# Performance work log

Hardware: AMD Instinct MI355X
Metric: run time of the kernel (lower is better)

The kernel has to match this reference:

```python
import jax, jax.numpy as jnp
import numpy as np

N_EMBD = 1024
N_HEAD = 16
HEAD_DIM = N_EMBD // N_HEAD  # 64
R = 8
D_STD = HEAD_DIM - R         # 56
BLOCK_SIZE = 2048
B, T = 2, 2048
NEG = -1e9


def setup_inputs() -> dict:
    key = jax.random.key(0)
    ks = jax.random.split(key, 8)
    x = jax.random.normal(ks[0], (B, T, N_EMBD), dtype=jnp.float32)
    Wqkv = jax.random.normal(ks[1], (3 * N_EMBD, N_EMBD), dtype=jnp.float32) * 0.02
    Wproj = jax.random.normal(ks[2], (N_EMBD, N_EMBD), dtype=jnp.float32) * 0.02
    W_recip = jax.random.normal(ks[3], (HEAD_DIM, R), dtype=jnp.float32) * 0.02
    # mixing weights must be positive (sqrt is taken); match init scale
    w_std = jnp.full((N_HEAD,), 0.5, dtype=jnp.float32)
    w_rec = jnp.full((N_HEAD,), 0.3, dtype=jnp.float32)  # > threshold -> all heads RA
    w_disc = jnp.full((N_HEAD,), 0.2, dtype=jnp.float32)
    d_bias = jax.random.normal(ks[4], (N_HEAD, BLOCK_SIZE), dtype=jnp.float32) * 0.02
    return {"x": x, "Wqkv": Wqkv, "Wproj": Wproj, "W_recip": W_recip,
            "w_std": w_std, "w_rec": w_rec, "w_disc": w_disc, "d_bias": d_bias}


def reference(x, Wqkv, Wproj, W_recip, w_std, w_rec, w_disc, d_bias):
    Bx, Tx, C = x.shape
    H, hd = N_HEAD, HEAD_DIM
    qkv = x @ Wqkv.T                                   # (B,T,3C)
    q, k, v = jnp.split(qkv, 3, axis=-1)
    def heads(t):
        return t.reshape(Bx, Tx, H, hd).transpose(0, 2, 1, 3)  # (B,H,T,hd)
    q, k, v = heads(q), heads(k), heads(v)
    q_low = jnp.einsum('bhtd,dr->bhtr', q, W_recip)    # (B,H,T,R)
    k_low = jnp.einsum('bhtd,dr->bhtr', k, W_recip)
    sw_std = jnp.sqrt(w_std)[None, :, None, None]
    sw_rec = jnp.sqrt(w_rec)[None, :, None, None]
    # cross augmentation: q side carries k_low, k side carries q_low
    q_aug = jnp.concatenate([sw_std * q[..., :D_STD], sw_rec * k_low], axis=-1)
    k_aug = jnp.concatenate([sw_std * k[..., :D_STD], sw_rec * q_low], axis=-1)
    scale = 1.0 / jnp.sqrt(jnp.asarray(hd, dtype=x.dtype))
    scores = jnp.einsum('bhqd,bhkd->bhqk', q_aug, k_aug) * scale
    # per-head learned bias over key positions, broadcast over queries
    bias = w_disc[None, :, None, None] * d_bias[:, :Tx][None, :, None, :]
    scores = scores + bias
    causal = jnp.tril(jnp.ones((Tx, Tx), dtype=bool))
    scores = jnp.where(causal[None, None], scores, NEG)
    attn = jax.nn.softmax(scores, axis=-1)
    out = jnp.einsum('bhqk,bhkd->bhqd', attn, v)       # (B,H,T,hd)
    out = out.transpose(0, 2, 1, 3).reshape(Bx, Tx, C)
    return out @ Wproj.T
```

## Files before the change

kernel.cpp:

```cpp
#include <hip/hip_runtime.h>
#include <math.h>

#define T_SEQ 2048
#define NH 16
#define HD 64
#define CEMB 1024
#define NEGINF -3.0e38f
#define LOG2E 1.4426950408889634f

typedef unsigned short ushort;
typedef unsigned int uint;
typedef __attribute__((ext_vector_type(8))) short short8;
typedef __attribute__((ext_vector_type(4))) float f32x4;

#if __has_builtin(__builtin_amdgcn_exp2f)
#define EXP2(x) __builtin_amdgcn_exp2f(x)
#else
#define EXP2(x) exp2f(x)
#endif

__device__ __forceinline__ float b2f(ushort h) {
    union { uint u; float f; } cv; cv.u = ((uint)h) << 16; return cv.f;
}
__device__ __forceinline__ ushort f2b(float f) {
    union { float f; uint u; } cv; cv.f = f;
    return (ushort)((cv.u + 0x7FFF + ((cv.u >> 16) & 1)) >> 16);
}
__device__ __forceinline__ ushort f2b_fast(float f) {
    union { float f; uint u; } cv; cv.f = f;
    return (ushort)((cv.u + 0x8000) >> 16);
}
__device__ __forceinline__ uint pack_bf16(float a, float b) {
    union { float f; uint u; } ua, ub; ua.f = a; ub.f = b;
    return __builtin_amdgcn_perm(ub.u + 0x8000u, ua.u + 0x8000u, 0x07060302u);
}
__device__ __forceinline__ void gl2lds16(const ushort* g, ushort* l) {
    __builtin_amdgcn_global_load_lds(
        (const __attribute__((address_space(1))) void*)g,
        (__attribute__((address_space(3))) void*)l, 16, 0, 0);
}

__global__ __launch_bounds__(256) void prep_kernel(
    const float* __restrict__ x, const float* __restrict__ Wqkv,
    const float* __restrict__ Wproj, const float* __restrict__ W_recip,
    const float* __restrict__ w_disc, const float* __restrict__ d_bias,
    ushort* __restrict__ xb, ushort* __restrict__ wqkvb,
    ushort* __restrict__ wprojb, float* __restrict__ bias_pre)
{
    const int bid = blockIdx.x;
    if (bid < 8192) {
        const float* src; ushort* dst; int off;
        if (bid < 4096)      { src = x;     dst = xb;     off = bid; }
        else if (bid < 7168) { src = Wqkv;  dst = wqkvb;  off = bid - 4096; }
        else                 { src = Wproj; dst = wprojb; off = bid - 7168; }
        const int i = (off * 256 + threadIdx.x) * 4;
        const float4 v = *(const float4*)&src[i];
        ushort4 o;
        o.x = f2b(v.x); o.y = f2b(v.y); o.z = f2b(v.z); o.w = f2b(v.w);
        *(ushort4*)&dst[i] = o;
        return;
    }
    if (bid >= 8224) {
        const int h = bid - 8224;
        const float wd = w_disc[h] * LOG2E;
        const int j = h * T_SEQ + threadIdx.x * 8;
        const float4 a = *(const float4*)&d_bias[j];
        const float4 c = *(const float4*)&d_bias[j + 4];
        float4 oa, oc;
        oa.x = a.x * wd; oa.y = a.y * wd; oa.z = a.z * wd; oa.w = a.w * wd;
        oc.x = c.x * wd; oc.y = c.y * wd; oc.z = c.z * wd; oc.w = c.w * wd;
        *(float4*)&bias_pre[j] = oa;
        *(float4*)&bias_pre[j + 4] = oc;
        return;
    }
    const int wb = bid - 8192;
    const int qk = wb >> 4, h = wb & 15;
    const int e0 = threadIdx.x * 4;
    f32x4 acc[8];
    #pragma unroll
    for (int r = 0; r < 8; ++r) acc[r] = (f32x4){0.f, 0.f, 0.f, 0.f};
    #pragma unroll 4
    for (int d = 0; d < 64; ++d) {
        const float4 xv = *(const float4*)&Wqkv[(size_t)(qk * 1024 + h * 64 + d) * 1024 + e0];
        #pragma unroll
        for (int r = 0; r < 8; ++r) {
            const float w = W_recip[d * 8 + r];
            acc[r][0] = fmaf(w, xv.x, acc[r][0]);
            acc[r][1] = fmaf(w, xv.y, acc[r][1]);
            acc[r][2] = fmaf(w, xv.z, acc[r][2]);
            acc[r][3] = fmaf(w, xv.w, acc[r][3]);
        }
    }
    #pragma unroll
    for (int r = 0; r < 8; ++r) {
        ushort4 o;
        o.x = f2b(acc[r][0]); o.y = f2b(acc[r][1]);
        o.z = f2b(acc[r][2]); o.w = f2b(acc[r][3]);
        *(ushort4*)&wqkvb[(size_t)(3072 + qk * 128 + h * 8 + r) * 1024 + e0] = o;
    }
}

#define GEMM_CORE(Aptr, Bptr, KDIM, SMEMN)                                     \
    __shared__ __align__(16) ushort SMEM[SMEMN];                               \
    ushort* const Asl = SMEM;                                                  \
    ushort* const Bsl = SMEM + 8192;                                           \
    const int row0 = blockIdx.x * 128;                                         \
    const int col0 = blockIdx.y * 128;                                         \
    const int tid = threadIdx.x;                                               \
    const int wave = tid >> 6, lane = tid & 63;                                \
    const int wm = wave >> 1, wn = wave & 1;                                   \
    const int quad = lane >> 4, lq = lane & 15;                                \
    const int l7 = lq & 7;                                                     \
    f32x4 acc[4][4];                                                           \
    _Pragma("unroll") for (int i = 0; i < 4; ++i)                              \
        _Pragma("unroll") for (int j = 0; j < 4; ++j)                          \
            acc[i][j] = (f32x4){0.f, 0.f, 0.f, 0.f};                           \
    for (int k0 = 0; k0 < (KDIM); k0 += 64) {                                  \
        _Pragma("unroll") for (int p = 0; p < 4; ++p) {                        \
            const int idx = p * 256 + tid;                                     \
            const int row = idx >> 3, slot = idx & 7;                          \
            const int kc = (slot ^ (row & 7)) << 3;                            \
            gl2lds16(&(Aptr)[(size_t)(row0 + row) * (KDIM) + k0 + kc], &Asl[idx * 8]); \
            gl2lds16(&(Bptr)[(size_t)(col0 + row) * (KDIM) + k0 + kc], &Bsl[idx * 8]); \
        }                                                                      \
        __syncthreads();                                                       \
        _Pragma("unroll") for (int ks = 0; ks < 2; ++ks) {                     \
            short8 af[4], bf[4];                                               \
            _Pragma("unroll") for (int i = 0; i < 4; ++i)                      \
                af[i] = *(const short8*)&Asl[(wm * 64 + i * 16 + lq) * 64 +    \
                                             (((ks * 4 + quad) ^ l7) << 3)];   \
            _Pragma("unroll") for (int j = 0; j < 4; ++j)                      \
                bf[j] = *(const short8*)&Bsl[(wn * 64 + j * 16 + lq) * 64 +    \
                                             (((ks * 4 + quad) ^ l7) << 3)];   \
            _Pragma("unroll") for (int i = 0; i < 4; ++i)                      \
                _Pragma("unroll") for (int j = 0; j < 4; ++j)                  \
                    acc[i][j] = __builtin_amdgcn_mfma_f32_16x16x32_bf16(       \
                        af[i], bf[j], acc[i][j], 0, 0, 0);                     \
        }                                                                      \
        __syncthreads();                                                       \
    }

__global__ __launch_bounds__(256, 4) void gemm_qkv_kernel(
    const ushort* __restrict__ A, const ushort* __restrict__ Bt,
    const float* __restrict__ w_std, const float* __restrict__ w_rec,
    ushort* __restrict__ qh, ushort* __restrict__ kh, ushort* __restrict__ vt)
{
    GEMM_CORE(A, Bt, 1024, 128 * 136)
    ushort* const Cs = SMEM;

    if (col0 >= 2048 && col0 < 3072) {
        #pragma unroll
        for (int j = 0; j < 4; ++j) {
            const int cc = col0 + wn * 64 + j * 16 + lq;
            const int h = (cc >> 6) & 15;
            const int d = cc & 63;
            #pragma unroll
            for (int i = 0; i < 4; ++i) {
                const int rr0 = row0 + wm * 64 + i * 16 + quad * 4;
                const int b = rr0 >> 11, t0 = rr0 & 2047;
                ushort4 pv;
                pv.x = f2b(acc[i][j][0]); pv.y = f2b(acc[i][j][1]);
                pv.z = f2b(acc[i][j][2]); pv.w = f2b(acc[i][j][3]);
                *(ushort4*)&vt[((((size_t)b * NH + h) * HD + d) * T_SEQ + t0)] = pv;
            }
        }
    } else if (col0 < 2048) {
        const bool isq = (col0 < 1024);
        #pragma unroll
        for (int j = 0; j < 4; ++j) {
            const int colc = wn * 64 + j * 16 + lq;
            const int h = ((col0 + colc) >> 6) & 15;
            const float sc = isq ? w_std[h] * (0.125f * LOG2E) : 1.0f;
            #pragma unroll
            for (int i = 0; i < 4; ++i)
                #pragma unroll
                for (int r = 0; r < 4; ++r)
                    Cs[(wm * 64 + i * 16 + quad * 4 + r) * 136 + colc] =
                        f2b(acc[i][j][r] * sc);
        }
        __syncthreads();
        ushort* dst = isq ? qh : kh;
        const int hbase = (col0 >> 6) & 15;
        #pragma unroll
        for (int rep = 0; rep < 8; ++rep) {
            const int id = rep * 256 + tid;
            const int row = id >> 4, chunk = id & 15;
            if ((chunk & 7) == 7) continue;
            const int h = hbase + (chunk >> 3);
            const int d = (chunk & 7) * 8;
            const int rr = row0 + row;
            const int b = rr >> 11, t = rr & 2047;
            const uint4 val = *(const uint4*)&Cs[row * 136 + chunk * 8];
            *(uint4*)&dst[((((size_t)b * NH + h) * T_SEQ + t) * HD + d)] = val;
        }
    } else {
        const bool isqlow = (col0 < 3200);
        #pragma unroll
        for (int j = 0; j < 4; ++j) {
            const int colc = wn * 64 + j * 16 + lq;
            const int h = colc >> 3;
            const float sc = isqlow ? 1.0f : w_rec[h] * (0.125f * LOG2E);
            #pragma unroll
            for (int i = 0; i < 4; ++i)
                #pragma unroll
                for (int r = 0; r < 4; ++r)
                    Cs[(wm * 64 + i * 16 + quad * 4 + r) * 136 + colc] =
                        f2b(acc[i][j][r] * sc);
        }
        __syncthreads();
        ushort* dst = isqlow ? kh : qh;
        #pragma unroll
        for (int rep = 0; rep < 8; ++rep) {
            const int id = rep * 256 + tid;
            const int row = id >> 4, h = id & 15;
            const int rr = row0 + row;
            const int b = rr >> 11, t = rr & 2047;
            const uint4 val = *(const uint4*)&Cs[row * 136 + h * 8];
            *(uint4*)&dst[((((size_t)b * NH + h) * T_SEQ + t) * HD + 56)] = val;
        }
    }
}

__global__ __launch_bounds__(256, 4) void gemm_proj_kernel(
    const ushort* __restrict__ A, const ushort* __restrict__ Bt,
    float* __restrict__ C)
{
    GEMM_CORE(A, Bt, 1024, 16384)
    #pragma unroll
    for (int i = 0; i < 4; ++i) {
        #pragma unroll
        for (int r = 0; r < 4; ++r) {
            const int rr = row0 + wm * 64 + i * 16 + quad * 4 + r;
            #pragma unroll
            for (int j = 0; j < 4; ++j) {
                const int cc = col0 + wn * 64 + j * 16 + lq;
                C[(size_t)rr * 1024 + cc] = acc[i][j][r];
            }
        }
    }
}

#define TILE_COMPUTE(bq, o4, lsum, qrow, NTL) do {                            \
    f32x4 s4[8];                                                              \
    _Pragma("unroll") for (int nt = 0; nt < (NTL); ++nt)                      \
        s4[nt] = *(const f32x4*)&bias_h[k0 + nt * 16 + quad * 4];             \
    _Pragma("unroll") for (int ks = 0; ks < 2; ++ks)                          \
        _Pragma("unroll") for (int nt = 0; nt < (NTL); ++nt) {                \
            const short8 ak = *(const short8*)                                \
                &Ks[(nt * 16 + lq) * 64 + (((ks * 4 + quad) ^ l7) << 3)];     \
            s4[nt] = __builtin_amdgcn_mfma_f32_16x16x32_bf16(                 \
                ak, (bq)[ks], s4[nt], 0, 0, 0);                               \
        }                                                                     \
    _Pragma("unroll") for (int nt = 0; nt < (NTL); ++nt) {                    \
        f32x4 sv = s4[nt];                                                    \
        const int kb = k0 + nt * 16 + quad * 4;                               \
        _Pragma("unroll") for (int r = 0; r < 4; ++r)                         \
            if (kb + r > (qrow)) sv[r] = NEGINF;                              \
        const float p0 = EXP2(sv[0]), p1 = EXP2(sv[1]);                       \
        const float p2 = EXP2(sv[2]), p3 = EXP2(sv[3]);                       \
        (lsum) += (p0 + p1) + (p2 + p3);                                      \
        const int pcol = (nt * 16 + quad * 4) ^ (l7 << 3);                    \
        uint2 pv; pv.x = pack_bf16(p0, p1); pv.y = pack_bf16(p2, p3);         \
        *(uint2*)&Ps[prow + pcol] = pv;                                       \
    }                                                                         \
    _Pragma("unroll") for (int ks = 0; ks < (NTL) / 2; ++ks) {                \
        const short8 bp = *(const short8*)                                    \
            &Ps[prow + ((ks * 32 + quad * 8) ^ (l7 << 3))];                   \
        _Pragma("unroll") for (int dt = 0; dt < 4; ++dt) {                    \
            const short8 av = *(const short8*)                                \
                &Vs[(dt * 16 + lq) * 128 + (((ks * 4 + quad) ^ lq) << 3)];    \
            (o4)[dt] = __builtin_amdgcn_mfma_f32_16x16x32_bf16(               \
                av, bp, (o4)[dt], 0, 0, 0);                                   \
        }                                                                     \
    }                                                                         \
} while (0)

__global__ __launch_bounds__(256, 2) void attn_kernel(
    const ushort* __restrict__ qa, const ushort* __restrict__ ka,
    const ushort* __restrict__ vt, const float* __restrict__ bias_pre,
    ushort* __restrict__ out)
{
    __shared__ __align__(16) ushort Qs[2 * 64 * 64];
    __shared__ __align__(16) ushort Ks[128 * 64];
    __shared__ __align__(16) ushort Ps[64 * 128];
    __shared__ __align__(16) ushort Vs[64 * 128];
    const int bh = blockIdx.x;
    const int qtA = blockIdx.y;
    const int qtB = 31 - blockIdx.y;
    const int h = bh & 15, b = bh >> 4;
    const int tid = threadIdx.x;
    const int wave = tid >> 6, lane = tid & 63;
    const int quad = lane >> 4, lq = lane & 15;
    const int l7 = lq & 7;
    const size_t base = (size_t)bh * T_SEQ * HD;

    #pragma unroll
    for (int rep = 0; rep < 2; ++rep) {
        const int idx = rep * 256 + tid;
        const int row = idx >> 3, slot = idx & 7;
        const int kc = (slot ^ (row & 7)) << 3;
        gl2lds16(&qa[base + (size_t)(qtA * 64 + row) * 64 + kc], &Qs[idx * 8]);
        gl2lds16(&qa[base + (size_t)(qtB * 64 + row) * 64 + kc], &Qs[4096 + idx * 8]);
    }
    __syncthreads();
    short8 bqA[2], bqB[2];
    #pragma unroll
    for (int ks = 0; ks < 2; ++ks) {
        const int off = (wave * 16 + lq) * 64 + (((ks * 4 + quad) ^ l7) << 3);
        bqA[ks] = *(const short8*)&Qs[off];
        bqB[ks] = *(const short8*)&Qs[4096 + off];
    }

    f32x4 o4A[4], o4B[4];
    #pragma unroll
    for (int dt = 0; dt < 4; ++dt) {
        o4A[dt] = (f32x4){0.f, 0.f, 0.f, 0.f};
        o4B[dt] = (f32x4){0.f, 0.f, 0.f, 0.f};
    }
    float lsumA = 0.f, lsumB = 0.f;
    const int qrowA = qtA * 64 + wave * 16 + lq;
    const int qrowB = qtB * 64 + wave * 16 + lq;
    const int prow = (wave * 16 + lq) * 128;
    const int nA = (qtA + 2) >> 1, nB = (qtB + 2) >> 1;
    const float* bias_h = &bias_pre[h * T_SEQ];

    for (int c = 0; c < nB; ++c) {
        const int k0 = c * 128;
        if (c) __syncthreads();
        #pragma unroll
        for (int rep = 0; rep < 4; ++rep) {
            const int idx = rep * 256 + tid;
            const int row = idx >> 3, slot = idx & 7;
            gl2lds16(&ka[base + (size_t)(k0 + row) * 64 + ((slot ^ (row & 7)) << 3)],
                     &Ks[idx * 8]);
        }
        #pragma unroll
        for (int rep = 0; rep < 4; ++rep) {
            const int idx = rep * 256 + tid;
            const int row = idx >> 4, slot = idx & 15;
            gl2lds16(&vt[base + (size_t)row * T_SEQ + k0 + ((slot ^ (row & 15)) << 3)],
                     &Vs[idx * 8]);
        }
        __syncthreads();

        if (c == nB - 1 && !(qtB & 1)) TILE_COMPUTE(bqB, o4B, lsumB, qrowB, 4);
        else                           TILE_COMPUTE(bqB, o4B, lsumB, qrowB, 8);
        if (c < nA) {
            if (c == nA - 1 && !(qtA & 1)) TILE_COMPUTE(bqA, o4A, lsumA, qrowA, 4);
            else                           TILE_COMPUTE(bqA, o4A, lsumA, qrowA, 8);
        }
    }

    lsumA += __shfl_xor(lsumA, 16, 64);
    lsumA += __shfl_xor(lsumA, 32, 64);
    lsumB += __shfl_xor(lsumB, 16, 64);
    lsumB += __shfl_xor(lsumB, 32, 64);
    const float invA = 1.0f / lsumA, invB = 1.0f / lsumB;
    const size_t obaseA = ((size_t)b * T_SEQ + qrowA) * CEMB + h * HD;
    const size_t obaseB = ((size_t)b * T_SEQ + qrowB) * CEMB + h * HD;
    #pragma unroll
    for (int dt = 0; dt < 4; ++dt) {
        ushort4 ov;
        ov.x = f2b_fast(o4A[dt][0] * invA);
        ov.y = f2b_fast(o4A[dt][1] * invA);
        ov.z = f2b_fast(o4A[dt][2] * invA);
        ov.w = f2b_fast(o4A[dt][3] * invA);
        *(ushort4*)&out[obaseA + dt * 16 + quad * 4] = ov;
        ushort4 ow;
        ow.x = f2b_fast(o4B[dt][0] * invB);
        ow.y = f2b_fast(o4B[dt][1] * invB);
        ow.z = f2b_fast(o4B[dt][2] * invB);
        ow.w = f2b_fast(o4B[dt][3] * invB);
        *(ushort4*)&out[obaseB + dt * 16 + quad * 4] = ow;
    }
}

extern "C" void kernel_launch(void* const* d_in, const int* in_sizes, int n_in,
                              void* d_out, int out_size, void* d_ws, size_t ws_size,
                              hipStream_t stream) {
    const float* x       = (const float*)d_in[0];
    const float* Wqkv    = (const float*)d_in[1];
    const float* Wproj   = (const float*)d_in[2];
    const float* W_recip = (const float*)d_in[3];
    const float* w_std   = (const float*)d_in[4];
    const float* w_rec   = (const float*)d_in[5];
    const float* w_disc  = (const float*)d_in[6];
    const float* d_bias  = (const float*)d_in[7];
    float* out = (float*)d_out;

    const size_t NX = (size_t)4096 * 1024;
    const size_t NWQKVX = (size_t)3328 * 1024;
    const size_t NWPROJ = (size_t)1024 * 1024;
    ushort* xb     = (ushort*)d_ws;
    ushort* wqkvb  = xb + NX;
    ushort* wprojb = wqkvb + NWQKVX;
    ushort* qh     = wprojb + NWPROJ;
    ushort* kh     = qh + NX;
    ushort* vt     = kh + NX;
    ushort* ao     = vt + NX;
    float*  bias_pre = (float*)(ao + NX);

    prep_kernel<<<8240, 256, 0, stream>>>(x, Wqkv, Wproj, W_recip, w_disc, d_bias,
                                          xb, wqkvb, wprojb, bias_pre);
    gemm_qkv_kernel<<<dim3(32, 26), 256, 0, stream>>>(xb, wqkvb, w_std, w_rec, qh, kh, vt);
    attn_kernel<<<dim3(32, 16), 256, 0, stream>>>(qh, kh, vt, bias_pre, ao);
    gemm_proj_kernel<<<dim3(32, 8), 256, 0, stream>>>(ao, wprojb, out);
}
```

Before: 190.7 us.

## Interleave dual query-tile attention compute, drop Q LDS staging, raise occupancy

Restructures the attention inner loop so both paired query tiles (A and B) share each K and V fragment read from LDS, interleaving their MFMAs. It adds s_setprio around the MFMA phases, loads Q directly from global into registers instead of staging through LDS, and reuses the K buffer for A's probabilities after a barrier. Removing the Q buffer frees LDS and launch bounds go from 2 to 3 blocks per SM. The costs are higher register pressure from two sets of score accumulators and one extra barrier per chunk.

```diff
diff --git a/kernel.cpp b/kernel.cpp
--- a/kernel.cpp
+++ b/kernel.cpp
@@ -240,19 +240,9 @@
     }
 }
 
-#define TILE_COMPUTE(bq, o4, lsum, qrow, NTL) do {                            \
-    f32x4 s4[8];                                                              \
-    _Pragma("unroll") for (int nt = 0; nt < (NTL); ++nt)                      \
-        s4[nt] = *(const f32x4*)&bias_h[k0 + nt * 16 + quad * 4];             \
-    _Pragma("unroll") for (int ks = 0; ks < 2; ++ks)                          \
-        _Pragma("unroll") for (int nt = 0; nt < (NTL); ++nt) {                \
-            const short8 ak = *(const short8*)                                \
-                &Ks[(nt * 16 + lq) * 64 + (((ks * 4 + quad) ^ l7) << 3)];     \
-            s4[nt] = __builtin_amdgcn_mfma_f32_16x16x32_bf16(                 \
-                ak, (bq)[ks], s4[nt], 0, 0, 0);                               \
-        }                                                                     \
+#define SOFTMAX_ROWS(sarr, NTL, qrow, lsum, Pdst) do {                        \
     _Pragma("unroll") for (int nt = 0; nt < (NTL); ++nt) {                    \
-        f32x4 sv = s4[nt];                                                    \
+        f32x4 sv = (sarr)[nt];                                                \
         const int kb = k0 + nt * 16 + quad * 4;                               \
         _Pragma("unroll") for (int r = 0; r < 4; ++r)                         \
             if (kb + r > (qrow)) sv[r] = NEGINF;                              \
@@ -261,29 +251,88 @@
         (lsum) += (p0 + p1) + (p2 + p3);                                      \
         const int pcol = (nt * 16 + quad * 4) ^ (l7 << 3);                    \
         uint2 pv; pv.x = pack_bf16(p0, p1); pv.y = pack_bf16(p2, p3);         \
-        *(uint2*)&Ps[prow + pcol] = pv;                                       \
+        *(uint2*)&(Pdst)[prow + pcol] = pv;                                   \
     }                                                                         \
+} while (0)
+
+#define CHUNK_DUAL(NTA) do {                                                  \
+    f32x4 sA[(NTA)], sB[8];                                                   \
+    _Pragma("unroll") for (int nt = 0; nt < 8; ++nt) {                        \
+        const f32x4 bv = *(const f32x4*)&bias_h[k0 + nt * 16 + quad * 4];     \
+        sB[nt] = bv;                                                          \
+        if (nt < (NTA)) sA[nt] = bv;                                          \
+    }                                                                         \
+    __builtin_amdgcn_s_setprio(1);                                            \
+    _Pragma("unroll") for (int ks = 0; ks < 2; ++ks)                          \
+        _Pragma("unroll") for (int nt = 0; nt < 8; ++nt) {                    \
+            const short8 ak = *(const short8*)                                \
+                &Ks[(nt * 16 + lq) * 64 + (((ks * 4 + quad) ^ l7) << 3)];     \
+            sB[nt] = __builtin_amdgcn_mfma_f32_16x16x32_bf16(                 \
+                ak, bqB[ks], sB[nt], 0, 0, 0);                                \
+            if (nt < (NTA))                                                   \
+                sA[nt] = __builtin_amdgcn_mfma_f32_16x16x32_bf16(             \
+                    ak, bqA[ks], sA[nt], 0, 0, 0);                            \
+        }                                                                     \
+    __builtin_amdgcn_s_setprio(0);                                            \
+    __syncthreads();        \
+    SOFTMAX_ROWS(sB, 8, qrowB, lsumB, Ps);                                    \
+    SOFTMAX_ROWS(sA, (NTA), qrowA, lsumA, PA);                                \
+    __builtin_amdgcn_s_setprio(1);                                            \
+    _Pragma("unroll") for (int ks = 0; ks < 4; ++ks) {                        \
+        const int poff = prow + ((ks * 32 + quad * 8) ^ (l7 << 3));           \
+        const short8 bpB = *(const short8*)&Ps[poff];                         \
+        short8 bpA = bpB;                                                     \
+        if (ks < (NTA) / 2) bpA = *(const short8*)&PA[poff];                  \
+        _Pragma("unroll") for (int dt = 0; dt < 4; ++dt) {                    \
+            const short8 av = *(const short8*)                                \
+                &Vs[(dt * 16 + lq) * 128 + (((ks * 4 + quad) ^ lq) << 3)];    \
+            o4B[dt] = __builtin_amdgcn_mfma_f32_16x16x32_bf16(                \
+                av, bpB, o4B[dt], 0, 0, 0);                                   \
+            if (ks < (NTA) / 2)                                               \
+                o4A[dt] = __builtin_amdgcn_mfma_f32_16x16x32_bf16(            \
+                    av, bpA, o4A[dt], 0, 0, 0);                               \
+        }                                                                     \
+    }                                                                         \
+    __builtin_amdgcn_s_setprio(0);                                            \
+} while (0)
+
+#define CHUNK_SINGLE(NTL) do {                                                \
+    f32x4 sB[(NTL)];                                                          \
+    _Pragma("unroll") for (int nt = 0; nt < (NTL); ++nt)                      \
+        sB[nt] = *(const f32x4*)&bias_h[k0 + nt * 16 + quad * 4];             \
+    __builtin_amdgcn_s_setprio(1);                                            \
+    _Pragma("unroll") for (int ks = 0; ks < 2; ++ks)                          \
+        _Pragma("unroll") for (int nt = 0; nt < (NTL); ++nt) {                \
+            const short8 ak = *(const short8*)                                \
+                &Ks[(nt * 16 + lq) * 64 + (((ks * 4 + quad) ^ l7) << 3)];     \
+            sB[nt] = __builtin_amdgcn_mfma_f32_16x16x32_bf16(                 \
+                ak, bqB[ks], sB[nt], 0, 0, 0);                                \
+        }                                                                     \
+    __builtin_amdgcn_s_setprio(0);                                            \
+    SOFTMAX_ROWS(sB, (NTL), qrowB, lsumB, Ps);                                \
+    __builtin_amdgcn_s_setprio(1);                                            \
     _Pragma("unroll") for (int ks = 0; ks < (NTL) / 2; ++ks) {                \
-        const short8 bp = *(const short8*)                                    \
+        const short8 bpB = *(const short8*)                                   \
             &Ps[prow + ((ks * 32 + quad * 8) ^ (l7 << 3))];                   \
         _Pragma("unroll") for (int dt = 0; dt < 4; ++dt) {                    \
             const short8 av = *(const short8*)                                \
                 &Vs[(dt * 16 + lq) * 128 + (((ks * 4 + quad) ^ lq) << 3)];    \
-            (o4)[dt] = __builtin_amdgcn_mfma_f32_16x16x32_bf16(               \
-                av, bp, (o4)[dt], 0, 0, 0);                                   \
+            o4B[dt] = __builtin_amdgcn_mfma_f32_16x16x32_bf16(                \
+                av, bpB, o4B[dt], 0, 0, 0);                                   \
         }                                                                     \
     }                                                                         \
+    __builtin_amdgcn_s_setprio(0);                                            \
 } while (0)
 
-__global__ __launch_bounds__(256, 2) void attn_kernel(
+__global__ __launch_bounds__(256, 3) void attn_kernel(
     const ushort* __restrict__ qa, const ushort* __restrict__ ka,
     const ushort* __restrict__ vt, const float* __restrict__ bias_pre,
     ushort* __restrict__ out)
 {
-    __shared__ __align__(16) ushort Qs[2 * 64 * 64];
     __shared__ __align__(16) ushort Ks[128 * 64];
     __shared__ __align__(16) ushort Ps[64 * 128];
     __shared__ __align__(16) ushort Vs[64 * 128];
+    ushort* const PA = Ks;
     const int bh = blockIdx.x;
     const int qtA = blockIdx.y;
     const int qtB = 31 - blockIdx.y;
@@ -294,21 +343,15 @@
     const int l7 = lq & 7;
     const size_t base = (size_t)bh * T_SEQ * HD;
 
-    #pragma unroll
-    for (int rep = 0; rep < 2; ++rep) {
-        const int idx = rep * 256 + tid;
-        const int row = idx >> 3, slot = idx & 7;
-        const int kc = (slot ^ (row & 7)) << 3;
-        gl2lds16(&qa[base + (size_t)(qtA * 64 + row) * 64 + kc], &Qs[idx * 8]);
-        gl2lds16(&qa[base + (size_t)(qtB * 64 + row) * 64 + kc], &Qs[4096 + idx * 8]);
-    }
-    __syncthreads();
+    const int qrowA = qtA * 64 + wave * 16 + lq;
+    const int qrowB = qtB * 64 + wave * 16 + lq;
+
     short8 bqA[2], bqB[2];
     #pragma unroll
     for (int ks = 0; ks < 2; ++ks) {
-        const int off = (wave * 16 + lq) * 64 + (((ks * 4 + quad) ^ l7) << 3);
-        bqA[ks] = *(const short8*)&Qs[off];
-        bqB[ks] = *(const short8*)&Qs[4096 + off];
+        const int dq = (ks * 4 + quad) * 8;
+        bqA[ks] = *(const short8*)&qa[base + (size_t)qrowA * 64 + dq];
+        bqB[ks] = *(const short8*)&qa[base + (size_t)qrowB * 64 + dq];
     }
 
     f32x4 o4A[4], o4B[4];
@@ -318,8 +361,6 @@
         o4B[dt] = (f32x4){0.f, 0.f, 0.f, 0.f};
     }
     float lsumA = 0.f, lsumB = 0.f;
-    const int qrowA = qtA * 64 + wave * 16 + lq;
-    const int qrowB = qtB * 64 + wave * 16 + lq;
     const int prow = (wave * 16 + lq) * 128;
     const int nA = (qtA + 2) >> 1, nB = (qtB + 2) >> 1;
     const float* bias_h = &bias_pre[h * T_SEQ];
@@ -343,11 +384,12 @@
         }
         __syncthreads();
 
-        if (c == nB - 1 && !(qtB & 1)) TILE_COMPUTE(bqB, o4B, lsumB, qrowB, 4);
-        else                           TILE_COMPUTE(bqB, o4B, lsumB, qrowB, 8);
         if (c < nA) {
-            if (c == nA - 1 && !(qtA & 1)) TILE_COMPUTE(bqA, o4A, lsumA, qrowA, 4);
-            else                           TILE_COMPUTE(bqA, o4A, lsumA, qrowA, 8);
+            if (c == nA - 1 && !(qtA & 1)) { CHUNK_DUAL(4); }
+            else                           { CHUNK_DUAL(8); }
+        } else {
+            if (c == nB - 1 && !(qtB & 1)) { CHUNK_SINGLE(4); }
+            else                           { CHUNK_SINGLE(8); }
         }
     }
 
```

Result: slower. 265.6 us (+39.3%).

## Double-buffer K/V tiles in attention and drop paired query-tile scheduling

Applied to the files above, without the earlier changes.

The attention kernel now handles one 64-row query tile per block, with a doubled grid. It double-buffers K and V chunks in LDS so the next chunk's global-to-LDS load overlaps compute on the current one, using manual vmcnt waits and raw barriers. Q is loaded straight from global into registers instead of staged through LDS, and s_setprio raises wave priority around the MFMA sections. The change gives up the paired short/long tile load balancing and uses more LDS per block, which can lower occupancy.

```diff
diff --git a/kernel.cpp b/kernel.cpp
--- a/kernel.cpp
+++ b/kernel.cpp
@@ -240,39 +240,67 @@
     }
 }
 
-#define TILE_COMPUTE(bq, o4, lsum, qrow, NTL) do {                            \
-    f32x4 s4[8];                                                              \
+#define STAGE_K(cc, dst) do {                                                 \
+    const int kk0 = (cc) * 128;                                               \
+    _Pragma("unroll") for (int rep = 0; rep < 4; ++rep) {                     \
+        const int idx = rep * 256 + tid;                                      \
+        const int row = idx >> 3, slot = idx & 7;                             \
+        gl2lds16(&ka[base + (size_t)(kk0 + row) * 64 +                        \
+                     ((slot ^ (row & 7)) << 3)], &(dst)[idx * 8]);            \
+    }                                                                         \
+} while (0)
+
+#define STAGE_V(cc, dst) do {                                                 \
+    const int kk0 = (cc) * 128;                                               \
+    _Pragma("unroll") for (int rep = 0; rep < 4; ++rep) {                     \
+        const int idx = rep * 256 + tid;                                      \
+        const int row = idx >> 4, slot = idx & 15;                            \
+        gl2lds16(&vt[base + (size_t)row * T_SEQ + kk0 +                       \
+                     ((slot ^ (row & 15)) << 3)], &(dst)[idx * 8]);           \
+    }                                                                         \
+} while (0)
+
+#define SOFTMAX_ROWS(sarr, NTL) do {                                          \
+    _Pragma("unroll") for (int nt = 0; nt < (NTL); ++nt) {                    \
+        f32x4 sv = (sarr)[nt];                                                \
+        const int kb = k0 + nt * 16 + quad * 4;                               \
+        _Pragma("unroll") for (int r = 0; r < 4; ++r)                         \
+            if (kb + r > qrow) sv[r] = NEGINF;                                \
+        const float p0 = EXP2(sv[0]), p1 = EXP2(sv[1]);                       \
+        const float p2 = EXP2(sv[2]), p3 = EXP2(sv[3]);                       \
+        lsum += (p0 + p1) + (p2 + p3);                                        \
+        const int pcol = (nt * 16 + quad * 4) ^ (l7 << 3);                    \
+        uint2 pv; pv.x = pack_bf16(p0, p1); pv.y = pack_bf16(p2, p3);         \
+        *(uint2*)&Ps[prow + pcol] = pv;                                       \
+    }                                                                         \
+} while (0)
+
+#define ATTN_CHUNK(NTL) do {                                                  \
+    f32x4 s4[(NTL)];                                                          \
     _Pragma("unroll") for (int nt = 0; nt < (NTL); ++nt)                      \
         s4[nt] = *(const f32x4*)&bias_h[k0 + nt * 16 + quad * 4];             \
+    __builtin_amdgcn_s_setprio(1);                                            \
     _Pragma("unroll") for (int ks = 0; ks < 2; ++ks)                          \
         _Pragma("unroll") for (int nt = 0; nt < (NTL); ++nt) {                \
             const short8 ak = *(const short8*)                                \
                 &Ks[(nt * 16 + lq) * 64 + (((ks * 4 + quad) ^ l7) << 3)];     \
             s4[nt] = __builtin_amdgcn_mfma_f32_16x16x32_bf16(                 \
-                ak, (bq)[ks], s4[nt], 0, 0, 0);                               \
+                ak, bq[ks], s4[nt], 0, 0, 0);                                 \
         }                                                                     \
-    _Pragma("unroll") for (int nt = 0; nt < (NTL); ++nt) {                    \
-        f32x4 sv = s4[nt];                                                    \
-        const int kb = k0 + nt * 16 + quad * 4;                               \
-        _Pragma("unroll") for (int r = 0; r < 4; ++r)                         \
-            if (kb + r > (qrow)) sv[r] = NEGINF;                              \
-        const float p0 = EXP2(sv[0]), p1 = EXP2(sv[1]);                       \
-        const float p2 = EXP2(sv[2]), p3 = EXP2(sv[3]);                       \
-        (lsum) += (p0 + p1) + (p2 + p3);                                      \
-        const int pcol = (nt * 16 + quad * 4) ^ (l7 << 3);                    \
-        uint2 pv; pv.x = pack_bf16(p0, p1); pv.y = pack_bf16(p2, p3);         \
-        *(uint2*)&Ps[prow + pcol] = pv;                                       \
-    }                                                                         \
+    __builtin_amdgcn_s_setprio(0);                                            \
+    SOFTMAX_ROWS(s4, (NTL));                                                  \
+    __builtin_amdgcn_s_setprio(1);                                            \
     _Pragma("unroll") for (int ks = 0; ks < (NTL) / 2; ++ks) {                \
         const short8 bp = *(const short8*)                                    \
             &Ps[prow + ((ks * 32 + quad * 8) ^ (l7 << 3))];                   \
         _Pragma("unroll") for (int dt = 0; dt < 4; ++dt) {                    \
             const short8 av = *(const short8*)                                \
                 &Vs[(dt * 16 + lq) * 128 + (((ks * 4 + quad) ^ lq) << 3)];    \
-            (o4)[dt] = __builtin_amdgcn_mfma_f32_16x16x32_bf16(               \
-                av, bp, (o4)[dt], 0, 0, 0);                                   \
+            o4[dt] = __builtin_amdgcn_mfma_f32_16x16x32_bf16(                 \
+                av, bp, o4[dt], 0, 0, 0);                                     \
         }                                                                     \
     }                                                                         \
+    __builtin_amdgcn_s_setprio(0);                                            \
 } while (0)
 
 __global__ __launch_bounds__(256, 2) void attn_kernel(
@@ -280,98 +308,68 @@
     const ushort* __restrict__ vt, const float* __restrict__ bias_pre,
     ushort* __restrict__ out)
 {
-    __shared__ __align__(16) ushort Qs[2 * 64 * 64];
-    __shared__ __align__(16) ushort Ks[128 * 64];
+    __shared__ __align__(16) ushort KbA[128 * 64];
+    __shared__ __align__(16) ushort KbB[128 * 64];
+    __shared__ __align__(16) ushort VbA[64 * 128];
+    __shared__ __align__(16) ushort VbB[64 * 128];
     __shared__ __align__(16) ushort Ps[64 * 128];
-    __shared__ __align__(16) ushort Vs[64 * 128];
     const int bh = blockIdx.x;
-    const int qtA = blockIdx.y;
-    const int qtB = 31 - blockIdx.y;
+    const int qt = 31 - blockIdx.y;
     const int h = bh & 15, b = bh >> 4;
     const int tid = threadIdx.x;
     const int wave = tid >> 6, lane = tid & 63;
     const int quad = lane >> 4, lq = lane & 15;
     const int l7 = lq & 7;
     const size_t base = (size_t)bh * T_SEQ * HD;
-
-    #pragma unroll
-    for (int rep = 0; rep < 2; ++rep) {
-        const int idx = rep * 256 + tid;
-        const int row = idx >> 3, slot = idx & 7;
-        const int kc = (slot ^ (row & 7)) << 3;
-        gl2lds16(&qa[base + (size_t)(qtA * 64 + row) * 64 + kc], &Qs[idx * 8]);
-        gl2lds16(&qa[base + (size_t)(qtB * 64 + row) * 64 + kc], &Qs[4096 + idx * 8]);
-    }
-    __syncthreads();
-    short8 bqA[2], bqB[2];
-    #pragma unroll
-    for (int ks = 0; ks < 2; ++ks) {
-        const int off = (wave * 16 + lq) * 64 + (((ks * 4 + quad) ^ l7) << 3);
-        bqA[ks] = *(const short8*)&Qs[off];
-        bqB[ks] = *(const short8*)&Qs[4096 + off];
-    }
-
-    f32x4 o4A[4], o4B[4];
-    #pragma unroll
-    for (int dt = 0; dt < 4; ++dt) {
-        o4A[dt] = (f32x4){0.f, 0.f, 0.f, 0.f};
-        o4B[dt] = (f32x4){0.f, 0.f, 0.f, 0.f};
-    }
-    float lsumA = 0.f, lsumB = 0.f;
-    const int qrowA = qtA * 64 + wave * 16 + lq;
-    const int qrowB = qtB * 64 + wave * 16 + lq;
+    const int qrow = qt * 64 + wave * 16 + lq;
     const int prow = (wave * 16 + lq) * 128;
-    const int nA = (qtA + 2) >> 1, nB = (qtB + 2) >> 1;
+    const int nc = (qt + 2) >> 1;
     const float* bias_h = &bias_pre[h * T_SEQ];
 
-    for (int c = 0; c < nB; ++c) {
+    short8 bq[2];
+    #pragma unroll
+    for (int ks = 0; ks < 2; ++ks)
+        bq[ks] = *(const short8*)&qa[base + (size_t)qrow * 64 + (ks * 4 + quad) * 8];
+
+    f32x4 o4[4];
+    #pragma unroll
+    for (int dt = 0; dt < 4; ++dt) o4[dt] = (f32x4){0.f, 0.f, 0.f, 0.f};
+    float lsum = 0.f;
+
+    STAGE_K(0, KbA);
+    STAGE_V(0, VbA);
+
+    for (int c = 0; c < nc; ++c) {
         const int k0 = c * 128;
-        if (c) __syncthreads();
-        #pragma unroll
-        for (int rep = 0; rep < 4; ++rep) {
-            const int idx = rep * 256 + tid;
-            const int row = idx >> 3, slot = idx & 7;
-            gl2lds16(&ka[base + (size_t)(k0 + row) * 64 + ((slot ^ (row & 7)) << 3)],
-                     &Ks[idx * 8]);
-        }
-        #pragma unroll
-        for (int rep = 0; rep < 4; ++rep) {
-            const int idx = rep * 256 + tid;
-            const int row = idx >> 4, slot = idx & 15;
-            gl2lds16(&vt[base + (size_t)row * T_SEQ + k0 + ((slot ^ (row & 15)) << 3)],
-                     &Vs[idx * 8]);
-        }
-        __syncthreads();
-
-        if (c == nB - 1 && !(qtB & 1)) TILE_COMPUTE(bqB, o4B, lsumB, qrowB, 4);
-        else                           TILE_COMPUTE(bqB, o4B, lsumB, qrowB, 8);
-        if (c < nA) {
-            if (c == nA - 1 && !(qtA & 1)) TILE_COMPUTE(bqA, o4A, lsumA, qrowA, 4);
-            else                           TILE_COMPUTE(bqA, o4A, lsumA, qrowA, 8);
-        }
-    }
-
-    lsumA += __shfl_xor(lsumA, 16, 64);
-    lsumA += __shfl_xor(lsumA, 32, 64);
-    lsumB += __shfl_xor(lsumB, 16, 64);
-    lsumB += __shfl_xor(lsumB, 32, 64);
-    const float invA = 1.0f / lsumA, invB = 1.0f / lsumB;
-    const size_t obaseA = ((size_t)b * T_SEQ + qrowA) * CEMB + h * HD;
-    const size_t obaseB = ((size_t)b * T_SEQ + qrowB) * CEMB + h * HD;
+        ushort* const Ks = (c & 1) ? KbB : KbA;
+        ushort* const Vs = (c & 1) ? VbB : VbA;
+        if (c + 1 < nc) {
+            if (c & 1) { STAGE_K(c + 1, KbA); STAGE_V(c + 1, VbA); }
+            else       { STAGE_K(c + 1, KbB); STAGE_V(c + 1, VbB); }
+            asm volatile("s_waitcnt vmcnt(8)" ::: "memory");
+        } else {
+            asm volatile("s_waitcnt vmcnt(0)" ::: "memory");
+        }
+        __builtin_amdgcn_s_barrier();
+        __builtin_amdgcn_sched_barrier(0);
+        if (c == nc - 1 && !(qt & 1)) { ATTN_CHUNK(4); }
+        else                          { ATTN_CHUNK(8); }
+        __builtin_amdgcn_sched_barrier(0);
+        __builtin_amdgcn_s_barrier();
+    }
+
+    lsum += __shfl_xor(lsum, 16, 64);
+    lsum += __shfl_xor(lsum, 32, 64);
+    const float inv = 1.0f / lsum;
+    const size_t obase = ((size_t)b * T_SEQ + qrow) * CEMB + h * HD;
     #pragma unroll
     for (int dt = 0; dt < 4; ++dt) {
         ushort4 ov;
-        ov.x = f2b_fast(o4A[dt][0] * invA);
-        ov.y = f2b_fast(o4A[dt][1] * invA);
-        ov.z = f2b_fast(o4A[dt][2] * invA);
-        ov.w = f2b_fast(o4A[dt][3] * invA);
-        *(ushort4*)&out[obaseA + dt * 16 + quad * 4] = ov;
-        ushort4 ow;
-        ow.x = f2b_fast(o4B[dt][0] * invB);
-        ow.y = f2b_fast(o4B[dt][1] * invB);
-        ow.z = f2b_fast(o4B[dt][2] * invB);
-        ow.w = f2b_fast(o4B[dt][3] * invB);
-        *(ushort4*)&out[obaseB + dt * 16 + quad * 4] = ow;
+        ov.x = f2b_fast(o4[dt][0] * inv);
+        ov.y = f2b_fast(o4[dt][1] * inv);
+        ov.z = f2b_fast(o4[dt][2] * inv);
+        ov.w = f2b_fast(o4[dt][3] * inv);
+        *(ushort4*)&out[obase + dt * 16 + quad * 4] = ov;
     }
 }
 
@@ -403,6 +401,6 @@
     prep_kernel<<<8240, 256, 0, stream>>>(x, Wqkv, Wproj, W_recip, w_disc, d_bias,
                                           xb, wqkvb, wprojb, bias_pre);
     gemm_qkv_kernel<<<dim3(32, 26), 256, 0, stream>>>(xb, wqkvb, w_std, w_rec, qh, kh, vt);
-    attn_kernel<<<dim3(32, 16), 256, 0, stream>>>(qh, kh, vt, bias_pre, ao);
+    attn_kernel<<<dim3(32, 32), 256, 0, stream>>>(qh, kh, vt, bias_pre, ao);
     gemm_proj_kernel<<<dim3(32, 8), 256, 0, stream>>>(ao, wprojb, out);
 }
```

Result: no change. 191.6 us (+0.5%).
